# Kernel optimization log

Hardware: AMD Instinct MI355X
Metric: run time of the kernel (lower is better)

Reference implementation:

```python
import jax, jax.numpy as jnp
import numpy as np

DIMS = 1024
HEADS = 16
DEPTH = DIMS // HEADS


def setup_inputs() -> dict:
    key = jax.random.key(0)
    kq, kk, kv = jax.random.split(key, 3)
    B, S = 2, 2048
    q = jax.random.normal(kq, (B, S, DIMS), dtype=jnp.float32)
    k = jax.random.normal(kk, (B, S, DIMS), dtype=jnp.float32)
    v = jax.random.normal(kv, (B, S, DIMS), dtype=jnp.float32)
    return {"q": q, "k": k, "v": v}


def _split_heads(x):
    # [B, S, dims] -> [B, heads, S, depth]
    b, s, _ = x.shape
    return x.reshape(b, s, HEADS, DEPTH).transpose(0, 2, 1, 3)


def reference(q, k, v):
    b, s, _ = q.shape
    qh = _split_heads(q)  # [b, h, sq, d]
    kh = _split_heads(k)  # [b, h, sk, d]
    vh = _split_heads(v)  # [b, h, sk, d]
    # keras.layers.Attention default: UNSCALED dot-product scores
    scores = jnp.einsum("bhqd,bhkd->bhqk", qh, kh)
    weights = jax.nn.softmax(scores, axis=-1)
    out = jnp.einsum("bhqk,bhkd->bhqd", weights, vh)
    # merge heads: [b, h, sq, d] -> [b, sq, dims]
    out = out.transpose(0, 2, 1, 3).reshape(b, s, DIMS)
    return out
```

## Files before the change

kernel.cpp:

```cpp
#include <hip/hip_runtime.h>

#define SEQ 2048
#define HEADS 16
#define DEPTH 64
#define DIMS 1024
#define LOG2E 1.44269504088896340736f

typedef _Float16 f16x8 __attribute__((ext_vector_type(8)));
typedef _Float16 f16x4 __attribute__((ext_vector_type(4)));
typedef __fp16 fp16v2 __attribute__((ext_vector_type(2)));
typedef float f32x4 __attribute__((ext_vector_type(4)));

__device__ __forceinline__ f32x4 mfma16(f16x8 a, f16x8 b, f32x4 c) {
  return __builtin_amdgcn_mfma_f32_16x16x32_f16(a, b, c, 0, 0, 0);
}

#if __has_builtin(__builtin_amdgcn_exp2f)
#define EXP2(x) __builtin_amdgcn_exp2f(x)
#else
#define EXP2(x) exp2f(x)
#endif

#define GLOAD_LDS(g, l)                                                        \
  __builtin_amdgcn_global_load_lds(                                            \
      (const __attribute__((address_space(1))) unsigned int*)(g),              \
      (__attribute__((address_space(3))) unsigned int*)(l), 16, 0, 0)

__global__ __launch_bounds__(256) void prep_k(const float* __restrict__ k,
                                              _Float16* __restrict__ kh) {
  int t = blockIdx.x * 256 + threadIdx.x;
  size_t flat = (size_t)t * 8;
  int b = (int)(flat >> 21);
  int rem = (int)(flat & ((1u << 21) - 1));
  int s = rem >> 10;
  int c = rem & 1023;
  int h = c >> 6;
  int d = c & 63;
  float4 a0 = *(const float4*)(k + flat);
  float4 a1 = *(const float4*)(k + flat + 4);
  float f[8] = {a0.x, a0.y, a0.z, a0.w, a1.x, a1.y, a1.z, a1.w};
  f16x8 th;
  #pragma unroll
  for (int j = 0; j < 8; ++j) th[j] = (_Float16)f[j];
  size_t o = ((size_t)(b * HEADS + h) * SEQ + s) * DEPTH + d;
  *(f16x8*)(kh + o) = th;
}

__global__ __launch_bounds__(256) void prep_v(const float* __restrict__ v,
                                              _Float16* __restrict__ vt) {
  int t = blockIdx.x * 256 + threadIdx.x;
  int d = t & 63;
  int sg = (t >> 6) & 255;
  int bh = t >> 14;
  int b = bh >> 4, h = bh & 15;
  int s0 = sg * 8;
  const float* src = v + ((size_t)(b * SEQ + s0)) * DIMS + h * DEPTH + d;
  _Float16* dst = vt + ((size_t)bh * DEPTH + d) * SEQ + s0;
  f16x8 tv;
  #pragma unroll
  for (int i = 0; i < 8; ++i) tv[i] = (_Float16)src[(size_t)i * DIMS];
  *(f16x8*)dst = tv;
}

__global__ __launch_bounds__(256, 4) void attn_fwd(
    const float* __restrict__ q, const _Float16* __restrict__ kh,
    const _Float16* __restrict__ vt, float* __restrict__ out) {
  __shared__ _Float16 Kl[2][64 * 64];
  __shared__ _Float16 Vl[2][64 * 64];
  __shared__ _Float16 Pl[4][16 * 64];

  const int tid = threadIdx.x;
  const int w = tid >> 6;
  const int l = tid & 63;
  const int lg = l >> 4;
  const int lr = l & 15;

  const int bid = blockIdx.x;
  const int wg = (bid & 7) * 128 + (bid >> 3);
  const int qt = wg & 31;
  const int bh = wg >> 5;
  const int b = bh >> 4;
  const int h = bh & 15;

  const int qb = qt * 64 + w * 16;
  const int hoff = h * DEPTH;
  const size_t kvoff = (size_t)bh * SEQ * DEPTH;

  f16x8 qf[2];
  {
    const float* gq = q + (size_t)(b * SEQ + qb + lr) * DIMS + hoff + 8 * lg;
    #pragma unroll
    for (int c = 0; c < 2; ++c) {
      float4 a0 = *(const float4*)(gq + 32 * c);
      float4 a1 = *(const float4*)(gq + 32 * c + 4);
      float f[8] = {a0.x, a0.y, a0.z, a0.w, a1.x, a1.y, a1.z, a1.w};
      f16x8 t;
      #pragma unroll
      for (int j = 0; j < 8; ++j) t[j] = (_Float16)(f[j] * LOG2E);
      qf[c] = t;
    }
  }

  const int srow = l >> 3;
  const int scol = ((l & 7) ^ srow) * 8;
  const _Float16* gk0 = kh + kvoff + (size_t)(16 * w + srow) * DEPTH + scol;
  const _Float16* gv0 = vt + kvoff + (size_t)(16 * w + srow) * SEQ + scol;
  _Float16* Pw = &Pl[w][0];

  f32x4 acc[4] = {};
  float mrow = -3e38f;
  float den = 0.f;

  const int x7 = lr & 7;
  int kch[2];
  #pragma unroll
  for (int c = 0; c < 2; ++c) kch[c] = ((4 * c + lg) ^ x7) * 8;

  auto stage = [&](int buf, int t) {
    const _Float16* gk = gk0 + (size_t)t * 64 * DEPTH;
    const _Float16* gv = gv0 + (size_t)t * 64;
    GLOAD_LDS(gk, &Kl[buf][(16 * w) * 64]);
    GLOAD_LDS(gk + 8 * DEPTH, &Kl[buf][(16 * w + 8) * 64]);
    GLOAD_LDS(gv, &Vl[buf][(16 * w) * 64]);
    GLOAD_LDS(gv + (size_t)8 * SEQ, &Vl[buf][(16 * w + 8) * 64]);
  };

  auto compute = [&](int buf) {
    f32x4 st[4] = {};
    __builtin_amdgcn_s_setprio(1);
    #pragma unroll
    for (int nt = 0; nt < 4; ++nt)
      #pragma unroll
      for (int c = 0; c < 2; ++c) {
        f16x8 kf = *(const f16x8*)&Kl[buf][(nt * 16 + lr) * 64 + kch[c]];
        st[nt] = mfma16(kf, qf[c], st[nt]);
      }
    __builtin_amdgcn_s_setprio(0);

    float pmax = st[0][0];
    #pragma unroll
    for (int nt = 0; nt < 4; ++nt)
      #pragma unroll
      for (int r = 0; r < 4; ++r) pmax = fmaxf(pmax, st[nt][r]);
    pmax = fmaxf(pmax, __shfl_xor(pmax, 16));
    pmax = fmaxf(pmax, __shfl_xor(pmax, 32));
    if (!__all(pmax - mrow <= 8.0f)) {
      float mnew = fmaxf(mrow, pmax);
      float sc = EXP2(mrow - mnew);
      mrow = mnew;
      den *= sc;
      #pragma unroll
      for (int r = 0; r < 4; ++r) {
        float scb = __shfl(sc, (l & 48) | (4 * lg + r));
        #pragma unroll
        for (int dt = 0; dt < 4; ++dt) acc[dt][r] *= scb;
      }
    }
    float p[4][4];
    float rs = 0.f;
    #pragma unroll
    for (int nt = 0; nt < 4; ++nt)
      #pragma unroll
      for (int r = 0; r < 4; ++r) {
        p[nt][r] = EXP2(st[nt][r] - mrow);
        rs += p[nt][r];
      }
    rs += __shfl_xor(rs, 16);
    rs += __shfl_xor(rs, 32);
    den += rs;

    #pragma unroll
    for (int nt = 0; nt < 4; ++nt) {
      union { fp16v2 h2[2]; f16x4 h4; } pu;
      pu.h2[0] = __builtin_amdgcn_cvt_pkrtz(p[nt][0], p[nt][1]);
      pu.h2[1] = __builtin_amdgcn_cvt_pkrtz(p[nt][2], p[nt][3]);
      const int chunk = (2 * nt + (lg >> 1)) ^ x7;
      *(f16x4*)&Pw[lr * 64 + chunk * 8 + (lg & 1) * 4] = pu.h4;
    }

    __builtin_amdgcn_s_setprio(1);
    #pragma unroll
    for (int ks = 0; ks < 2; ++ks) {
      f16x8 pf = *(const f16x8*)&Pw[lr * 64 + kch[ks]];
      #pragma unroll
      for (int dt = 0; dt < 4; ++dt) {
        f16x8 vf = *(const f16x8*)&Vl[buf][(dt * 16 + lr) * 64 + kch[ks]];
        acc[dt] = mfma16(pf, vf, acc[dt]);
      }
    }
    __builtin_amdgcn_s_setprio(0);
  };

  stage(0, 0);
  __syncthreads();
  for (int kt = 0; kt < SEQ / 64; kt += 2) {
    stage(1, kt + 1);
    compute(0);
    __syncthreads();
    if (kt + 2 < SEQ / 64) stage(0, kt + 2);
    compute(1);
    __syncthreads();
  }

  float rden[4];
  #pragma unroll
  for (int r = 0; r < 4; ++r)
    rden[r] = 1.0f / __shfl(den, (l & 48) | (4 * lg + r));
  #pragma unroll
  for (int dt = 0; dt < 4; ++dt)
    #pragma unroll
    for (int r = 0; r < 4; ++r) {
      const int row = qb + 4 * lg + r;
      out[(size_t)(b * SEQ + row) * DIMS + hoff + dt * 16 + lr] =
          acc[dt][r] * rden[r];
    }
}

extern "C" void kernel_launch(void* const* d_in, const int* in_sizes, int n_in,
                              void* d_out, int out_size, void* d_ws, size_t ws_size,
                              hipStream_t stream) {
  const float* q = (const float*)d_in[0];
  const float* k = (const float*)d_in[1];
  const float* v = (const float*)d_in[2];
  float* out = (float*)d_out;

  const size_t tsz = (size_t)2 * HEADS * SEQ * DEPTH;
  _Float16* khf = (_Float16*)d_ws;
  _Float16* vtp = khf + tsz;

  prep_k<<<2048, 256, 0, stream>>>(k, khf);
  prep_v<<<2048, 256, 0, stream>>>(v, vtp);
  attn_fwd<<<1024, 256, 0, stream>>>(q, khf, vtp, out);
}
```

Before: 77.73 us.

## Process two 16-row query tiles per wave to reuse K/V fragments

Each wave now handles 32 query rows instead of 16, so each block covers 128 queries and the grid is halved to 512 blocks. Every K and V fragment read from LDS feeds two MFMAs, which halves LDS traffic and global K/V staging per query. The cost is twice the accumulator and score registers, so the launch-bounds occupancy hint drops from 4 to 2 blocks, and the smaller grid may leave the 256 CUs less evenly loaded.

Result: no change. 76.68 us (-1.3%).

```diff
diff --git a/kernel.cpp b/kernel.cpp
--- a/kernel.cpp
+++ b/kernel.cpp
@@ -62,12 +62,12 @@
   *(f16x8*)dst = tv;
 }
 
-__global__ __launch_bounds__(256, 4) void attn_fwd(
+__global__ __launch_bounds__(256, 2) void attn_fwd(
     const float* __restrict__ q, const _Float16* __restrict__ kh,
     const _Float16* __restrict__ vt, float* __restrict__ out) {
   __shared__ _Float16 Kl[2][64 * 64];
   __shared__ _Float16 Vl[2][64 * 64];
-  __shared__ _Float16 Pl[4][16 * 64];
+  __shared__ _Float16 Pl[4][32 * 64];
 
   const int tid = threadIdx.x;
   const int w = tid >> 6;
@@ -76,19 +76,21 @@
   const int lr = l & 15;
 
   const int bid = blockIdx.x;
-  const int wg = (bid & 7) * 128 + (bid >> 3);
-  const int qt = wg & 31;
-  const int bh = wg >> 5;
+  const int wg = (bid & 7) * 64 + (bid >> 3);
+  const int qt = wg & 15;
+  const int bh = wg >> 4;
   const int b = bh >> 4;
   const int h = bh & 15;
 
-  const int qb = qt * 64 + w * 16;
+  const int qb = qt * 128 + w * 32;
   const int hoff = h * DEPTH;
   const size_t kvoff = (size_t)bh * SEQ * DEPTH;
 
-  f16x8 qf[2];
-  {
-    const float* gq = q + (size_t)(b * SEQ + qb + lr) * DIMS + hoff + 8 * lg;
+  f16x8 qf[2][2];
+  #pragma unroll
+  for (int mt = 0; mt < 2; ++mt) {
+    const float* gq =
+        q + (size_t)(b * SEQ + qb + mt * 16 + lr) * DIMS + hoff + 8 * lg;
     #pragma unroll
     for (int c = 0; c < 2; ++c) {
       float4 a0 = *(const float4*)(gq + 32 * c);
@@ -97,7 +99,7 @@
       f16x8 t;
       #pragma unroll
       for (int j = 0; j < 8; ++j) t[j] = (_Float16)(f[j] * LOG2E);
-      qf[c] = t;
+      qf[mt][c] = t;
     }
   }
 
@@ -107,9 +109,9 @@
   const _Float16* gv0 = vt + kvoff + (size_t)(16 * w + srow) * SEQ + scol;
   _Float16* Pw = &Pl[w][0];
 
-  f32x4 acc[4] = {};
-  float mrow = -3e38f;
-  float den = 0.f;
+  f32x4 acc[2][4] = {};
+  float mrow[2] = {-3e38f, -3e38f};
+  float den[2] = {0.f, 0.f};
 
   const int x7 = lr & 7;
   int kch[2];
@@ -126,66 +128,68 @@
   };
 
   auto compute = [&](int buf) {
-    f32x4 st[4] = {};
+    f32x4 st[2][4] = {};
     __builtin_amdgcn_s_setprio(1);
     #pragma unroll
     for (int nt = 0; nt < 4; ++nt)
       #pragma unroll
       for (int c = 0; c < 2; ++c) {
         f16x8 kf = *(const f16x8*)&Kl[buf][(nt * 16 + lr) * 64 + kch[c]];
-        st[nt] = mfma16(kf, qf[c], st[nt]);
+        st[0][nt] = mfma16(kf, qf[0][c], st[0][nt]);
+        st[1][nt] = mfma16(kf, qf[1][c], st[1][nt]);
       }
     __builtin_amdgcn_s_setprio(0);
 
-    float pmax = st[0][0];
-    #pragma unroll
-    for (int nt = 0; nt < 4; ++nt)
-      #pragma unroll
-      for (int r = 0; r < 4; ++r) pmax = fmaxf(pmax, st[nt][r]);
-    pmax = fmaxf(pmax, __shfl_xor(pmax, 16));
-    pmax = fmaxf(pmax, __shfl_xor(pmax, 32));
-    if (!__all(pmax - mrow <= 8.0f)) {
-      float mnew = fmaxf(mrow, pmax);
-      float sc = EXP2(mrow - mnew);
-      mrow = mnew;
-      den *= sc;
-      #pragma unroll
-      for (int r = 0; r < 4; ++r) {
-        float scb = __shfl(sc, (l & 48) | (4 * lg + r));
+    #pragma unroll
+    for (int mt = 0; mt < 2; ++mt) {
+      float pmax = st[mt][0][0];
+      #pragma unroll
+      for (int nt = 0; nt < 4; ++nt)
         #pragma unroll
-        for (int dt = 0; dt < 4; ++dt) acc[dt][r] *= scb;
-      }
+        for (int r = 0; r < 4; ++r) pmax = fmaxf(pmax, st[mt][nt][r]);
+      pmax = fmaxf(pmax, __shfl_xor(pmax, 16));
+      pmax = fmaxf(pmax, __shfl_xor(pmax, 32));
+      if (!__all(pmax - mrow[mt] <= 8.0f)) {
+        float mnew = fmaxf(mrow[mt], pmax);
+        float sc = EXP2(mrow[mt] - mnew);
+        mrow[mt] = mnew;
+        den[mt] *= sc;
+        #pragma unroll
+        for (int r = 0; r < 4; ++r) {
+          float scb = __shfl(sc, (l & 48) | (4 * lg + r));
+          #pragma unroll
+          for (int dt = 0; dt < 4; ++dt) acc[mt][dt][r] *= scb;
+        }
+      }
+      float rs = 0.f;
+      #pragma unroll
+      for (int nt = 0; nt < 4; ++nt) {
+        float p0 = EXP2(st[mt][nt][0] - mrow[mt]);
+        float p1 = EXP2(st[mt][nt][1] - mrow[mt]);
+        float p2 = EXP2(st[mt][nt][2] - mrow[mt]);
+        float p3 = EXP2(st[mt][nt][3] - mrow[mt]);
+        rs += (p0 + p1) + (p2 + p3);
+        union { fp16v2 h2[2]; f16x4 h4; } pu;
+        pu.h2[0] = __builtin_amdgcn_cvt_pkrtz(p0, p1);
+        pu.h2[1] = __builtin_amdgcn_cvt_pkrtz(p2, p3);
+        const int chunk = (2 * nt + (lg >> 1)) ^ x7;
+        *(f16x4*)&Pw[(mt * 16 + lr) * 64 + chunk * 8 + (lg & 1) * 4] = pu.h4;
+      }
+      rs += __shfl_xor(rs, 16);
+      rs += __shfl_xor(rs, 32);
+      den[mt] += rs;
     }
-    float p[4][4];
-    float rs = 0.f;
-    #pragma unroll
-    for (int nt = 0; nt < 4; ++nt)
-      #pragma unroll
-      for (int r = 0; r < 4; ++r) {
-        p[nt][r] = EXP2(st[nt][r] - mrow);
-        rs += p[nt][r];
-      }
-    rs += __shfl_xor(rs, 16);
-    rs += __shfl_xor(rs, 32);
-    den += rs;
-
-    #pragma unroll
-    for (int nt = 0; nt < 4; ++nt) {
-      union { fp16v2 h2[2]; f16x4 h4; } pu;
-      pu.h2[0] = __builtin_amdgcn_cvt_pkrtz(p[nt][0], p[nt][1]);
-      pu.h2[1] = __builtin_amdgcn_cvt_pkrtz(p[nt][2], p[nt][3]);
-      const int chunk = (2 * nt + (lg >> 1)) ^ x7;
-      *(f16x4*)&Pw[lr * 64 + chunk * 8 + (lg & 1) * 4] = pu.h4;
-    }
 
     __builtin_amdgcn_s_setprio(1);
     #pragma unroll
     for (int ks = 0; ks < 2; ++ks) {
-      f16x8 pf = *(const f16x8*)&Pw[lr * 64 + kch[ks]];
+      f16x8 pf0 = *(const f16x8*)&Pw[(0 * 16 + lr) * 64 + kch[ks]];
+      f16x8 pf1 = *(const f16x8*)&Pw[(1 * 16 + lr) * 64 + kch[ks]];
       #pragma unroll
       for (int dt = 0; dt < 4; ++dt) {
         f16x8 vf = *(const f16x8*)&Vl[buf][(dt * 16 + lr) * 64 + kch[ks]];
-        acc[dt] = mfma16(pf, vf, acc[dt]);
+        acc[0][dt] = mfma16(pf0, vf, acc[0][dt]);
+        acc[1][dt] = mfma16(pf1, vf, acc[1][dt]);
       }
     }
     __builtin_amdgcn_s_setprio(0);
@@ -202,18 +206,21 @@
     __syncthreads();
   }
 
-  float rden[4];
-  #pragma unroll
-  for (int r = 0; r < 4; ++r)
-    rden[r] = 1.0f / __shfl(den, (l & 48) | (4 * lg + r));
-  #pragma unroll
-  for (int dt = 0; dt < 4; ++dt)
-    #pragma unroll
-    for (int r = 0; r < 4; ++r) {
-      const int row = qb + 4 * lg + r;
-      out[(size_t)(b * SEQ + row) * DIMS + hoff + dt * 16 + lr] =
-          acc[dt][r] * rden[r];
-    }
+  #pragma unroll
+  for (int mt = 0; mt < 2; ++mt) {
+    float rden[4];
+    #pragma unroll
+    for (int r = 0; r < 4; ++r)
+      rden[r] = 1.0f / __shfl(den[mt], (l & 48) | (4 * lg + r));
+    #pragma unroll
+    for (int dt = 0; dt < 4; ++dt)
+      #pragma unroll
+      for (int r = 0; r < 4; ++r) {
+        const int row = qb + mt * 16 + 4 * lg + r;
+        out[(size_t)(b * SEQ + row) * DIMS + hoff + dt * 16 + lr] =
+            acc[mt][dt][r] * rden[r];
+      }
+  }
 }
 
 extern "C" void kernel_launch(void* const* d_in, const int* in_sizes, int n_in,
@@ -230,5 +237,5 @@
 
   prep_k<<<2048, 256, 0, stream>>>(k, khf);
   prep_v<<<2048, 256, 0, stream>>>(v, vtp);
-  attn_fwd<<<1024, 256, 0, stream>>>(q, khf, vtp, out);
-}
+  attn_fwd<<<512, 256, 0, stream>>>(q, khf, vtp, out);
+}
```

## Switch attention to 32x32x16 MFMA with register-resident P via permlane32 swap

Applied to the files above, without the earlier changes.

Reworks the attention kernel to use 32x32x16 MFMA tiles, so each wave handles 32 query rows and a workgroup covers 128 queries. The probabilities are repacked into MFMA A-operands in registers with v_permlane32_swap instead of round-tripping through LDS, which removes the P shared buffer and its stores and loads. The grid is halved, launch bounds drop to 2 waves per SIMD, and the K and V prep kernels are merged into one launch. The cost is higher register pressure and fewer workgroups in flight.

New measurement: 72.57 us. -6.6%, faster.

```diff
diff --git a/kernel.cpp b/kernel.cpp
--- a/kernel.cpp
+++ b/kernel.cpp
@@ -7,12 +7,11 @@
 #define LOG2E 1.44269504088896340736f
 
 typedef _Float16 f16x8 __attribute__((ext_vector_type(8)));
-typedef _Float16 f16x4 __attribute__((ext_vector_type(4)));
 typedef __fp16 fp16v2 __attribute__((ext_vector_type(2)));
-typedef float f32x4 __attribute__((ext_vector_type(4)));
-
-__device__ __forceinline__ f32x4 mfma16(f16x8 a, f16x8 b, f32x4 c) {
-  return __builtin_amdgcn_mfma_f32_16x16x32_f16(a, b, c, 0, 0, 0);
+typedef float f32x16 __attribute__((ext_vector_type(16)));
+
+__device__ __forceinline__ f32x16 mfma32(f16x8 a, f16x8 b, f32x16 c) {
+  return __builtin_amdgcn_mfma_f32_32x32x16_f16(a, b, c, 0, 0, 0);
 }
 
 #if __has_builtin(__builtin_amdgcn_exp2f)
@@ -21,78 +20,85 @@
 #define EXP2(x) exp2f(x)
 #endif
 
+__device__ __forceinline__ unsigned pkbits(float a, float b) {
+  union { fp16v2 h; unsigned u; } cv;
+  cv.h = __builtin_amdgcn_cvt_pkrtz(a, b);
+  return cv.u;
+}
+
 #define GLOAD_LDS(g, l)                                                        \
   __builtin_amdgcn_global_load_lds(                                            \
       (const __attribute__((address_space(1))) unsigned int*)(g),              \
       (__attribute__((address_space(3))) unsigned int*)(l), 16, 0, 0)
 
-__global__ __launch_bounds__(256) void prep_k(const float* __restrict__ k,
-                                              _Float16* __restrict__ kh) {
-  int t = blockIdx.x * 256 + threadIdx.x;
-  size_t flat = (size_t)t * 8;
-  int b = (int)(flat >> 21);
-  int rem = (int)(flat & ((1u << 21) - 1));
-  int s = rem >> 10;
-  int c = rem & 1023;
-  int h = c >> 6;
-  int d = c & 63;
-  float4 a0 = *(const float4*)(k + flat);
-  float4 a1 = *(const float4*)(k + flat + 4);
-  float f[8] = {a0.x, a0.y, a0.z, a0.w, a1.x, a1.y, a1.z, a1.w};
-  f16x8 th;
-  #pragma unroll
-  for (int j = 0; j < 8; ++j) th[j] = (_Float16)f[j];
-  size_t o = ((size_t)(b * HEADS + h) * SEQ + s) * DEPTH + d;
-  *(f16x8*)(kh + o) = th;
-}
-
-__global__ __launch_bounds__(256) void prep_v(const float* __restrict__ v,
-                                              _Float16* __restrict__ vt) {
-  int t = blockIdx.x * 256 + threadIdx.x;
-  int d = t & 63;
-  int sg = (t >> 6) & 255;
-  int bh = t >> 14;
-  int b = bh >> 4, h = bh & 15;
-  int s0 = sg * 8;
-  const float* src = v + ((size_t)(b * SEQ + s0)) * DIMS + h * DEPTH + d;
-  _Float16* dst = vt + ((size_t)bh * DEPTH + d) * SEQ + s0;
-  f16x8 tv;
-  #pragma unroll
-  for (int i = 0; i < 8; ++i) tv[i] = (_Float16)src[(size_t)i * DIMS];
-  *(f16x8*)dst = tv;
-}
-
-__global__ __launch_bounds__(256, 4) void attn_fwd(
+__global__ __launch_bounds__(256) void prep_kv(const float* __restrict__ k,
+                                               const float* __restrict__ v,
+                                               _Float16* __restrict__ khf,
+                                               _Float16* __restrict__ vtp) {
+  const int bid = blockIdx.x;
+  if (bid < 2048) {
+    int t = bid * 256 + threadIdx.x;
+    size_t flat = (size_t)t * 8;
+    int b = (int)(flat >> 21);
+    int rem = (int)(flat & ((1u << 21) - 1));
+    int s = rem >> 10;
+    int c = rem & 1023;
+    int h = c >> 6;
+    int d = c & 63;
+    float4 a0 = *(const float4*)(k + flat);
+    float4 a1 = *(const float4*)(k + flat + 4);
+    float f[8] = {a0.x, a0.y, a0.z, a0.w, a1.x, a1.y, a1.z, a1.w};
+    f16x8 th;
+    #pragma unroll
+    for (int j = 0; j < 8; ++j) th[j] = (_Float16)f[j];
+    size_t o = ((size_t)(b * HEADS + h) * SEQ + s) * DEPTH + d;
+    *(f16x8*)(khf + o) = th;
+  } else {
+    int t = (bid - 2048) * 256 + threadIdx.x;
+    int d = t & 63;
+    int sg = (t >> 6) & 255;
+    int bh = t >> 14;
+    int b = bh >> 4, h = bh & 15;
+    int s0 = sg * 8;
+    const float* src = v + ((size_t)(b * SEQ + s0)) * DIMS + h * DEPTH + d;
+    _Float16* dst = vtp + ((size_t)bh * DEPTH + d) * SEQ + s0;
+    f16x8 tv;
+    #pragma unroll
+    for (int i = 0; i < 8; ++i) tv[i] = (_Float16)src[(size_t)i * DIMS];
+    *(f16x8*)dst = tv;
+  }
+}
+
+__global__ __launch_bounds__(256, 2) void attn_fwd(
     const float* __restrict__ q, const _Float16* __restrict__ kh,
     const _Float16* __restrict__ vt, float* __restrict__ out) {
   __shared__ _Float16 Kl[2][64 * 64];
   __shared__ _Float16 Vl[2][64 * 64];
-  __shared__ _Float16 Pl[4][16 * 64];
 
   const int tid = threadIdx.x;
   const int w = tid >> 6;
   const int l = tid & 63;
-  const int lg = l >> 4;
-  const int lr = l & 15;
+  const int q32 = l & 31;
+  const int hi = l >> 5;
 
   const int bid = blockIdx.x;
-  const int wg = (bid & 7) * 128 + (bid >> 3);
-  const int qt = wg & 31;
-  const int bh = wg >> 5;
+  const int wg = (bid & 7) * 64 + (bid >> 3);
+  const int qt = wg & 15;
+  const int bh = wg >> 4;
   const int b = bh >> 4;
   const int h = bh & 15;
 
-  const int qb = qt * 64 + w * 16;
+  const int qb = qt * 128 + w * 32;
   const int hoff = h * DEPTH;
   const size_t kvoff = (size_t)bh * SEQ * DEPTH;
 
-  f16x8 qf[2];
+  f16x8 qf[4];
   {
-    const float* gq = q + (size_t)(b * SEQ + qb + lr) * DIMS + hoff + 8 * lg;
-    #pragma unroll
-    for (int c = 0; c < 2; ++c) {
-      float4 a0 = *(const float4*)(gq + 32 * c);
-      float4 a1 = *(const float4*)(gq + 32 * c + 4);
+    const float* gq = q + (size_t)(b * SEQ + qb + q32) * DIMS + hoff + 8 * hi;
+    #pragma unroll
+    for (int c = 0; c < 4; ++c) {
+      float4 a0 = *(const float4*)(gq + 16 * c);
+      float4 a1 = *(const float4*)(gq + 16 * c + 4);
       float f[8] = {a0.x, a0.y, a0.z, a0.w, a1.x, a1.y, a1.z, a1.w};
       f16x8 t;
       #pragma unroll
@@ -105,16 +111,15 @@
   const int scol = ((l & 7) ^ srow) * 8;
   const _Float16* gk0 = kh + kvoff + (size_t)(16 * w + srow) * DEPTH + scol;
   const _Float16* gv0 = vt + kvoff + (size_t)(16 * w + srow) * SEQ + scol;
-  _Float16* Pw = &Pl[w][0];
-
-  f32x4 acc[4] = {};
+
+  const int x7 = q32 & 7;
+  int off[4];
+  #pragma unroll
+  for (int i = 0; i < 4; ++i) off[i] = ((2 * i + hi) ^ x7) * 8;
+
+  f32x16 acc0 = {}, acc1 = {};
   float mrow = -3e38f;
   float den = 0.f;
-
-  const int x7 = lr & 7;
-  int kch[2];
-  #pragma unroll
-  for (int c = 0; c < 2; ++c) kch[c] = ((4 * c + lg) ^ x7) * 8;
 
   auto stage = [&](int buf, int t) {
     const _Float16* gk = gk0 + (size_t)t * 64 * DEPTH;
@@ -126,73 +131,77 @@
   };
 
   auto compute = [&](int buf) {
-    f32x4 st[4] = {};
+    f32x16 st0 = {}, st1 = {};
     __builtin_amdgcn_s_setprio(1);
     #pragma unroll
-    for (int nt = 0; nt < 4; ++nt)
-      #pragma unroll
-      for (int c = 0; c < 2; ++c) {
-        f16x8 kf = *(const f16x8*)&Kl[buf][(nt * 16 + lr) * 64 + kch[c]];
-        st[nt] = mfma16(kf, qf[c], st[nt]);
-      }
+    for (int c = 0; c < 4; ++c) {
+      f16x8 kf0 = *(const f16x8*)&Kl[buf][q32 * 64 + off[c]];
+      f16x8 kf1 = *(const f16x8*)&Kl[buf][(32 + q32) * 64 + off[c]];
+      st0 = mfma32(kf0, qf[c], st0);
+      st1 = mfma32(kf1, qf[c], st1);
+    }
     __builtin_amdgcn_s_setprio(0);
 
-    float pmax = st[0][0];
-    #pragma unroll
-    for (int nt = 0; nt < 4; ++nt)
-      #pragma unroll
-      for (int r = 0; r < 4; ++r) pmax = fmaxf(pmax, st[nt][r]);
-    pmax = fmaxf(pmax, __shfl_xor(pmax, 16));
-    pmax = fmaxf(pmax, __shfl_xor(pmax, 32));
-    if (!__all(pmax - mrow <= 8.0f)) {
-      float mnew = fmaxf(mrow, pmax);
+    float mx = fmaxf(st0[0], st1[0]);
+    #pragma unroll
+    for (int r = 1; r < 16; ++r) mx = fmaxf(mx, fmaxf(st0[r], st1[r]));
+    if (!__all(mx - mrow <= 8.0f)) {
+      mx = fmaxf(mx, __shfl_xor(mx, 32));
+      float mnew = fmaxf(mrow, mx);
       float sc = EXP2(mrow - mnew);
       mrow = mnew;
       den *= sc;
       #pragma unroll
-      for (int r = 0; r < 4; ++r) {
-        float scb = __shfl(sc, (l & 48) | (4 * lg + r));
-        #pragma unroll
-        for (int dt = 0; dt < 4; ++dt) acc[dt][r] *= scb;
+      for (int r = 0; r < 16; ++r) {
+        const int crow = (r & 3) + 8 * (r >> 2) + 4 * hi;
+        float scb = __shfl(sc, crow);
+        acc0[r] *= scb;
+        acc1[r] *= scb;
       }
     }
-    float p[4][4];
+    float p0[16], p1[16];
     float rs = 0.f;
     #pragma unroll
-    for (int nt = 0; nt < 4; ++nt)
-      #pragma unroll
-      for (int r = 0; r < 4; ++r) {
-        p[nt][r] = EXP2(st[nt][r] - mrow);
-        rs += p[nt][r];
-      }
-    rs += __shfl_xor(rs, 16);
+    for (int r = 0; r < 16; ++r) {
+      p0[r] = EXP2(st0[r] - mrow);
+      p1[r] = EXP2(st1[r] - mrow);
+      rs += p0[r] + p1[r];
+    }
     rs += __shfl_xor(rs, 32);
     den += rs;
 
-    #pragma unroll
-    for (int nt = 0; nt < 4; ++nt) {
-      union { fp16v2 h2[2]; f16x4 h4; } pu;
-      pu.h2[0] = __builtin_amdgcn_cvt_pkrtz(p[nt][0], p[nt][1]);
-      pu.h2[1] = __builtin_amdgcn_cvt_pkrtz(p[nt][2], p[nt][3]);
-      const int chunk = (2 * nt + (lg >> 1)) ^ x7;
-      *(f16x4*)&Pw[lr * 64 + chunk * 8 + (lg & 1) * 4] = pu.h4;
-    }
+    f16x8 pa[4];
+    auto mkpa = [&](const float* pp, f16x8* dst) {
+      #pragma unroll
+      for (int sl = 0; sl < 2; ++sl) {
+        unsigned x0 = pkbits(pp[8 * sl + 0], pp[8 * sl + 1]);
+        unsigned x1 = pkbits(pp[8 * sl + 2], pp[8 * sl + 3]);
+        unsigned y0 = pkbits(pp[8 * sl + 4], pp[8 * sl + 5]);
+        unsigned y1 = pkbits(pp[8 * sl + 6], pp[8 * sl + 7]);
+        asm("v_permlane32_swap_b32 %0, %1" : "+v"(x0), "+v"(y0));
+        asm("v_permlane32_swap_b32 %0, %1" : "+v"(x1), "+v"(y1));
+        union { unsigned u[4]; f16x8 v; } pu;
+        pu.u[0] = x0; pu.u[1] = x1; pu.u[2] = y0; pu.u[3] = y1;
+        dst[sl] = pu.v;
+      }
+    };
+    mkpa(p0, &pa[0]);
+    mkpa(p1, &pa[2]);
 
     __builtin_amdgcn_s_setprio(1);
     #pragma unroll
-    for (int ks = 0; ks < 2; ++ks) {
-      f16x8 pf = *(const f16x8*)&Pw[lr * 64 + kch[ks]];
-      #pragma unroll
-      for (int dt = 0; dt < 4; ++dt) {
-        f16x8 vf = *(const f16x8*)&Vl[buf][(dt * 16 + lr) * 64 + kch[ks]];
-        acc[dt] = mfma16(pf, vf, acc[dt]);
-      }
+    for (int s = 0; s < 4; ++s) {
+      f16x8 vf0 = *(const f16x8*)&Vl[buf][q32 * 64 + off[s]];
+      f16x8 vf1 = *(const f16x8*)&Vl[buf][(32 + q32) * 64 + off[s]];
+      acc0 = mfma32(pa[s], vf0, acc0);
+      acc1 = mfma32(pa[s], vf1, acc1);
     }
     __builtin_amdgcn_s_setprio(0);
   };
 
   stage(0, 0);
   __syncthreads();
+  #pragma unroll 1
   for (int kt = 0; kt < SEQ / 64; kt += 2) {
     stage(1, kt + 1);
     compute(0);
@@ -202,18 +211,15 @@
     __syncthreads();
   }
 
-  float rden[4];
   #pragma unroll
-  for (int r = 0; r < 4; ++r)
-    rden[r] = 1.0f / __shfl(den, (l & 48) | (4 * lg + r));
-  #pragma unroll
-  for (int dt = 0; dt < 4; ++dt)
-    #pragma unroll
-    for (int r = 0; r < 4; ++r) {
-      const int row = qb + 4 * lg + r;
-      out[(size_t)(b * SEQ + row) * DIMS + hoff + dt * 16 + lr] =
-          acc[dt][r] * rden[r];
-    }
+  for (int r = 0; r < 16; ++r) {
+    const int crow = (r & 3) + 8 * (r >> 2) + 4 * hi;
+    float dn = __shfl(den, crow);
+    float rden = 1.0f / dn;
+    float* po = out + (size_t)(b * SEQ + qb + crow) * DIMS + hoff;
+    po[q32] = acc0[r] * rden;
+    po[32 + q32] = acc1[r] * rden;
+  }
 }
 
 extern "C" void kernel_launch(void* const* d_in, const int* in_sizes, int n_in,
@@ -228,7 +234,6 @@
   _Float16* khf = (_Float16*)d_ws;
   _Float16* vtp = khf + tsz;
 
-  prep_k<<<2048, 256, 0, stream>>>(k, khf);
-  prep_v<<<2048, 256, 0, stream>>>(v, vtp);
-  attn_fwd<<<1024, 256, 0, stream>>>(q, khf, vtp, out);
-}
+  prep_kv<<<4096, 256, 0, stream>>>(k, v, khf, vtp);
+  attn_fwd<<<512, 256, 0, stream>>>(q, khf, vtp, out);
+}
```
